# Kernel tuning notes

Measured on AMD Instinct MI355X. Metric: run time of the kernel, lower is better.

## Reference

```python
import jax, jax.numpy as jnp
import numpy as np
from jax import lax

B, V, C, D, H, W = 1, 5, 32, 48, 128, 160
RATIO = 8


def setup_inputs() -> dict:
    key = jax.random.key(0)
    k1, k2, k3 = jax.random.split(key, 3)
    features = jax.random.normal(k1, (V, B, C, H, W), jnp.float32)
    # proj_matrices[b, v, 0] = 4x4 extrinsic, proj_matrices[b, v, 1, :3, :3] = intrinsic K
    f = 200.0
    K = np.array([[f, 0.0, W / 2.0], [0.0, f, H / 2.0], [0.0, 0.0, 1.0]], np.float32)
    proj = np.zeros((B, V, 2, 4, 4), np.float32)
    for v in range(V):
        E = np.eye(4, dtype=np.float32)
        E[0, 3] = 2.0 * v  # horizontal baseline per source view
        proj[:, v, 0] = E
        P1 = np.eye(4, dtype=np.float32)
        P1[:3, :3] = K
        proj[:, v, 1] = P1
    proj_matrices = jnp.asarray(proj)
    depth_values = jnp.broadcast_to(jnp.linspace(425.0, 935.0, D, dtype=jnp.float32), (B, D))
    mask = jax.random.normal(k2, (B, 9 * RATIO * RATIO, H, W), jnp.float32)
    W_reg = jax.random.normal(k3, (1, C, 3, 3, 3), jnp.float32) * 0.05
    return {"features": features, "proj_matrices": proj_matrices,
            "depth_values": depth_values, "mask": mask, "W_reg": W_reg}


def _combine(p):
    # p: [B,2,4,4] -> K @ E[:3,:4] written into top 3 rows of extrinsic (as in source)
    top = jnp.einsum('bij,bjk->bik', p[:, 1, :3, :3], p[:, 0, :3, :4])
    return p[:, 0].at[:, :3, :4].set(top)


def _bilinear_sample(src, x, y):
    # src [B,C,H,W]; x,y [B,P] pixel coords; zeros padding, align_corners=True
    Bs, Cs, Hs, Ws = src.shape
    x0 = jnp.floor(x)
    y0 = jnp.floor(y)
    wx = x - x0
    wy = y - y0
    src_flat = src.reshape(Bs, Cs, Hs * Ws)

    def gather(xi, yi, w):
        valid = (xi >= 0) & (xi <= Ws - 1) & (yi >= 0) & (yi <= Hs - 1)
        xi_c = jnp.clip(xi, 0, Ws - 1).astype(jnp.int32)
        yi_c = jnp.clip(yi, 0, Hs - 1).astype(jnp.int32)
        idx = (yi_c * Ws + xi_c)[:, None, :]
        vals = jnp.take_along_axis(src_flat, jnp.broadcast_to(idx, (Bs, Cs, idx.shape[-1])), axis=2)
        return vals * (w * valid)[:, None, :]

    return (gather(x0, y0, (1 - wx) * (1 - wy)) + gather(x0 + 1, y0, wx * (1 - wy))
            + gather(x0, y0 + 1, (1 - wx) * wy) + gather(x0 + 1, y0 + 1, wx * wy))


def _homo_warp(src_fea, src_proj, ref_proj, depth_values):
    # faithful homo_warping2: project ref pixel grid at each depth hypothesis into src view
    Bs, Cs, Hs, Ws = src_fea.shape
    Dd = depth_values.shape[1]
    proj = jnp.einsum('bij,bjk->bik', src_proj, jnp.linalg.inv(ref_proj))
    rot = proj[:, :3, :3]
    trans = proj[:, :3, 3]
    ys, xs = jnp.meshgrid(jnp.arange(Hs, dtype=src_fea.dtype), jnp.arange(Ws, dtype=src_fea.dtype), indexing='ij')
    xyz = jnp.stack([xs.ravel(), ys.ravel(), jnp.ones(Hs * Ws, dtype=src_fea.dtype)])  # [3,HW]
    rot_xyz = jnp.einsum('bij,jp->bip', rot, xyz)  # [B,3,HW]
    pts = rot_xyz[:, :, None, :] * depth_values[:, None, :, None] + trans[:, :, None, None]  # [B,3,D,HW]
    gx = pts[:, 0] / pts[:, 2]
    gy = pts[:, 1] / pts[:, 2]
    warped = _bilinear_sample(src_fea, gx.reshape(Bs, -1), gy.reshape(Bs, -1))
    return warped.reshape(Bs, Cs, Dd, Hs, Ws)


def _convex_upsample(depth, mask, r):
    # depth [N,1,H,W], mask [N,9*r*r,H,W] -> [N, r*H, r*W]
    N, _, Hh, Ww = depth.shape
    m = jax.nn.softmax(mask.reshape(N, 1, 9, r, r, Hh, Ww), axis=2)
    dp = jnp.pad(depth, ((0, 0), (0, 0), (1, 1), (1, 1)))
    nb = jnp.stack([dp[:, :, dy:dy + Hh, dx:dx + Ww] for dy in range(3) for dx in range(3)], axis=2)
    up = jnp.sum(m * nb[:, :, :, None, None], axis=2)  # [N,1,r,r,H,W]
    up = up.transpose(0, 1, 4, 2, 5, 3)  # [N,1,H,r,W,r]
    return up.reshape(N, r * Hh, r * Ww)


def reference(features, proj_matrices, depth_values, mask, W_reg):
    num_views = features.shape[0]
    Dd = depth_values.shape[1]
    ref_proj = _combine(proj_matrices[:, 0])
    # variance cost-volume accumulation over views (ref volume broadcast along D)
    vsum = features[0][:, :, None, :, :]
    vsq = vsum ** 2
    for v in range(1, num_views):
        src_proj = _combine(proj_matrices[:, v])
        wv = _homo_warp(features[v], src_proj, ref_proj, depth_values)
        vsum = vsum + wv
        vsq = vsq + wv * wv
    variance = vsq / num_views - (vsum / num_views) ** 2  # [B,C,D,H,W]
    # cost regularization stand-in: 3x3x3 conv C->1, SAME padding
    pre = lax.conv_general_dilated(variance, W_reg, (1, 1, 1), 'SAME',
                                   dimension_numbers=('NCDHW', 'OIDHW', 'NCDHW'))[:, 0]
    prob = jax.nn.softmax(pre, axis=1)  # [B,D,H,W]
    depth = jnp.sum(prob * depth_values[:, :, None, None], axis=1)  # [B,H,W]
    # photometric confidence (no-grad path): sliding sum of 4 along D, pad (1,2)
    pd = jnp.pad(prob, ((0, 0), (1, 2), (0, 0), (0, 0)))
    sum4 = pd[:, 0:Dd] + pd[:, 1:Dd + 1] + pd[:, 2:Dd + 2] + pd[:, 3:Dd + 3]
    di = jnp.sum(prob * jnp.arange(Dd, dtype=prob.dtype)[None, :, None, None], axis=1).astype(jnp.int32)
    di = jnp.clip(di, 0, Dd - 1)
    conf = jax.lax.stop_gradient(jnp.take_along_axis(sum4, di[:, None], axis=1)[:, 0])
    depth_up = _convex_upsample(depth[:, None], mask, RATIO)
    return (depth_up, depth, conf)
```

## Files before the change

### kernel.cpp

```cpp
#include <hip/hip_runtime.h>
#include <hip/hip_bf16.h>


#define NV 5
#define NC 32
#define ND 48
#define NH 128
#define NW 160
#define HW (NH * NW)
#define DHW (ND * HW)

typedef __attribute__((ext_vector_type(2))) float f32x2;

#define OFF_M      0
#define OFF_WF     256
#define OFF_DEPTHF 4096
#define OFF_PRE    86016
#define OFF_WV     4018176

__global__ void k_setup(const float* __restrict__ proj,
                        const float* __restrict__ wreg,
                        float* __restrict__ M, float* __restrict__ wf) {
  if (threadIdx.x != 0) return;
  double P[NV][2][4][4];
  for (int v = 0; v < NV; ++v)
    for (int m = 0; m < 2; ++m)
      for (int i = 0; i < 4; ++i)
        for (int j = 0; j < 4; ++j)
          P[v][m][i][j] = (double)proj[((v * 2 + m) * 4 + i) * 4 + j];
  double C[NV][4][4];
  for (int v = 0; v < NV; ++v) {
    for (int i = 0; i < 4; ++i)
      for (int j = 0; j < 4; ++j) C[v][i][j] = P[v][0][i][j];
    for (int i = 0; i < 3; ++i)
      for (int j = 0; j < 4; ++j) {
        double s = 0.0;
        for (int k = 0; k < 3; ++k) s += P[v][1][i][k] * P[v][0][k][j];
        C[v][i][j] = s;
      }
  }
  double a[4][8];
  for (int i = 0; i < 4; ++i)
    for (int j = 0; j < 4; ++j) { a[i][j] = C[0][i][j]; a[i][j + 4] = (i == j) ? 1.0 : 0.0; }
  for (int col = 0; col < 4; ++col) {
    int piv = col; double best = fabs(a[col][col]);
    for (int r = col + 1; r < 4; ++r) { double v = fabs(a[r][col]); if (v > best) { best = v; piv = r; } }
    if (piv != col)
      for (int j = 0; j < 8; ++j) { double t = a[col][j]; a[col][j] = a[piv][j]; a[piv][j] = t; }
    double pv = a[col][col];
    for (int j = 0; j < 8; ++j) a[col][j] /= pv;
    for (int r = 0; r < 4; ++r) if (r != col) {
      double f = a[r][col];
      for (int j = 0; j < 8; ++j) a[r][j] -= f * a[col][j];
    }
  }
  double inv[4][4];
  for (int i = 0; i < 4; ++i)
    for (int j = 0; j < 4; ++j) inv[i][j] = a[i][j + 4];
  for (int v = 1; v < NV; ++v) {
    float* m = M + (v - 1) * 12;
    for (int i = 0; i < 3; ++i) {
      double r[4] = {0, 0, 0, 0};
      for (int k = 0; k < 4; ++k) {
        double cv = C[v][i][k];
        for (int j = 0; j < 4; ++j) r[j] += cv * inv[k][j];
      }
      m[i * 3 + 0] = (float)r[0]; m[i * 3 + 1] = (float)r[1]; m[i * 3 + 2] = (float)r[2];
      m[9 + i] = (float)r[3];
    }
  }
  for (int c = 0; c < NC; ++c) {
    for (int t = 0; t < 27; ++t) wf[c * 28 + t] = wreg[c * 27 + t];
    wf[c * 28 + 27] = 0.f;
  }
}

__global__ __launch_bounds__(256) void k_warpvar(
    const float* __restrict__ feat,
    const float* __restrict__ depthv,
    const float* __restrict__ M,
    const float* __restrict__ wf,
    __hip_bfloat16* __restrict__ WV)
{
  int idx = blockIdx.x * 256 + threadIdx.x;
  int x = idx % NW;
  int t1 = idx / NW;
  int y = t1 % NH;
  int d = t1 / NH;
  float xf = (float)x, yf = (float)y;
  float df = depthv[d];

  int   cidx[16];
  float cw[16];
#pragma unroll
  for (int v = 0; v < 4; ++v) {
    const float* m = M + v * 12;
    float rx = m[0] * xf + m[1] * yf + m[2];
    float ry = m[3] * xf + m[4] * yf + m[5];
    float rz = m[6] * xf + m[7] * yf + m[8];
    float px = rx * df + m[9];
    float py = ry * df + m[10];
    float pz = rz * df + m[11];
    float gx = px / pz;
    float gy = py / pz;
    float x0 = floorf(gx), y0 = floorf(gy);
    float wx = gx - x0, wy = gy - y0;
    float cxs[2] = {x0, x0 + 1.f}, cys[2] = {y0, y0 + 1.f};
    float wxs[2] = {1.f - wx, wx}, wys[2] = {1.f - wy, wy};
#pragma unroll
    for (int cy = 0; cy < 2; ++cy)
#pragma unroll
      for (int cx = 0; cx < 2; ++cx) {
        float fx = cxs[cx], fy = cys[cy];
        bool valid = (fx >= 0.f) && (fx <= (float)(NW - 1)) &&
                     (fy >= 0.f) && (fy <= (float)(NH - 1));
        float fxc = fminf(fmaxf(fx, 0.f), (float)(NW - 1));
        float fyc = fminf(fmaxf(fy, 0.f), (float)(NH - 1));
        int xi = (int)fxc, yi = (int)fyc;
        cidx[v * 4 + cy * 2 + cx] = yi * NW + xi;
        cw[v * 4 + cy * 2 + cx] = wxs[cx] * wys[cy] * (valid ? 1.f : 0.f);
      }
  }

  int pix = y * NW + x;
  f32x2 wv[14];
#pragma unroll
  for (int u = 0; u < 14; ++u) wv[u] = (f32x2){0.f, 0.f};

#pragma unroll
  for (int c = 0; c < NC; ++c) {
    float f0 = feat[c * HW + pix];
    float vs = f0, vq = f0 * f0;
#pragma unroll
    for (int v = 0; v < 4; ++v) {
      const float* fv = feat + ((v + 1) * NC + c) * HW;
      float val = cw[v * 4 + 0] * fv[cidx[v * 4 + 0]]
                + cw[v * 4 + 1] * fv[cidx[v * 4 + 1]]
                + cw[v * 4 + 2] * fv[cidx[v * 4 + 2]]
                + cw[v * 4 + 3] * fv[cidx[v * 4 + 3]];
      vs += val;
      vq += val * val;
    }
    float var = vq * 0.2f - (vs * 0.2f) * (vs * 0.2f);
    const f32x2* wrow = (const f32x2*)(wf + c * 28);
    f32x2 vv; vv.x = var; vv.y = var;
#pragma unroll
    for (int u = 0; u < 14; ++u) wv[u] += wrow[u] * vv;
  }

#pragma unroll
  for (int u = 0; u < 14; ++u) {
    int t0 = 2 * u;
    WV[t0 * DHW + idx] = __float2bfloat16(wv[u].x);
    if (t0 + 1 < 27) WV[(t0 + 1) * DHW + idx] = __float2bfloat16(wv[u].y);
  }
}

__global__ __launch_bounds__(256) void k_conv(const __hip_bfloat16* __restrict__ WV,
                                              float* __restrict__ pre) {
  int idx = blockIdx.x * 256 + threadIdx.x;
  int x = idx % NW;
  int t1 = idx / NW;
  int y = t1 % NH;
  int d = t1 / NH;
  float acc = 0.f;
#pragma unroll
  for (int dd = 0; dd < 3; ++dd) {
    int dp = d + dd - 1;
    bool dok = (dp >= 0) && (dp < ND);
    int dpc = min(max(dp, 0), ND - 1);
#pragma unroll
    for (int i = 0; i < 3; ++i) {
      int yp = y + i - 1;
      bool yok = (yp >= 0) && (yp < NH);
      int ypc = min(max(yp, 0), NH - 1);
#pragma unroll
      for (int j = 0; j < 3; ++j) {
        int xp = x + j - 1;
        bool xok = (xp >= 0) && (xp < NW);
        int xpc = min(max(xp, 0), NW - 1);
        int t = dd * 9 + i * 3 + j;
        float v = __bfloat162float(WV[t * DHW + dpc * HW + ypc * NW + xpc]);
        acc += (dok && yok && xok) ? v : 0.f;
      }
    }
  }
  pre[idx] = acc;
}

__global__ __launch_bounds__(256) void k_softmax(const float* __restrict__ pre,
                                                 const float* __restrict__ depthv,
                                                 float* __restrict__ depthf,
                                                 float* __restrict__ out_depth,
                                                 float* __restrict__ out_conf) {
  int p = blockIdx.x * 256 + threadIdx.x;
  float pr[ND];
  float m = -1e30f;
#pragma unroll
  for (int d = 0; d < ND; ++d) { pr[d] = pre[d * HW + p]; m = fmaxf(m, pr[d]); }
  float s = 0.f;
#pragma unroll
  for (int d = 0; d < ND; ++d) { pr[d] = expf(pr[d] - m); s += pr[d]; }
  float inv = 1.f / s;
  float dep = 0.f, ti = 0.f;
#pragma unroll
  for (int d = 0; d < ND; ++d) {
    float prob = pr[d] * inv;
    pr[d] = prob;
    dep += prob * depthv[d];
    ti += prob * (float)d;
  }
  int di = (int)ti;
  di = di < 0 ? 0 : (di > ND - 1 ? ND - 1 : di);
  float conf = 0.f;
#pragma unroll
  for (int d = 0; d < ND; ++d)
    conf += (d >= di - 1 && d <= di + 2) ? pr[d] : 0.f;
  depthf[p] = dep;
  out_depth[p] = dep;
  out_conf[p] = conf;
}

__global__ __launch_bounds__(256) void k_upsample(const float* __restrict__ mask,
                                                  const float* __restrict__ depthf,
                                                  float* __restrict__ out) {
  int idx = blockIdx.x * 256 + threadIdx.x;
  int fx = idx % (NW * 8);
  int fy = idx / (NW * 8);
  int x = fx >> 3, dx = fx & 7;
  int y = fy >> 3, dy = fy & 7;
  float mv[9];
  float mmax = -1e30f;
#pragma unroll
  for (int k = 0; k < 9; ++k) {
    mv[k] = mask[((k * 8 + dy) * 8 + dx) * HW + y * NW + x];
    mmax = fmaxf(mmax, mv[k]);
  }
  float s = 0.f;
#pragma unroll
  for (int k = 0; k < 9; ++k) { mv[k] = expf(mv[k] - mmax); s += mv[k]; }
  float acc = 0.f;
#pragma unroll
  for (int k = 0; k < 9; ++k) {
    int ky = y + k / 3 - 1;
    int kx = x + k % 3 - 1;
    bool ok = (ky >= 0) && (ky < NH) && (kx >= 0) && (kx < NW);
    int kyc = min(max(ky, 0), NH - 1);
    int kxc = min(max(kx, 0), NW - 1);
    float dv = depthf[kyc * NW + kxc];
    acc += mv[k] * (ok ? dv : 0.f);
  }
  out[idx] = acc / s;
}

extern "C" void kernel_launch(void* const* d_in, const int* in_sizes, int n_in,
                              void* d_out, int out_size, void* d_ws, size_t ws_size,
                              hipStream_t stream) {
  const float* feat   = (const float*)d_in[0];
  const float* proj   = (const float*)d_in[1];
  const float* depthv = (const float*)d_in[2];
  const float* mask   = (const float*)d_in[3];
  const float* wreg   = (const float*)d_in[4];

  char* ws = (char*)d_ws;
  float* M       = (float*)(ws + OFF_M);
  float* wf      = (float*)(ws + OFF_WF);
  float* depthf  = (float*)(ws + OFF_DEPTHF);
  float* pre     = (float*)(ws + OFF_PRE);
  __hip_bfloat16* WV = (__hip_bfloat16*)(ws + OFF_WV);

  float* out = (float*)d_out;
  float* out_depth = out + (NH * 8) * (NW * 8);
  float* out_conf  = out_depth + HW;

  k_setup<<<1, 64, 0, stream>>>(proj, wreg, M, wf);
  k_warpvar<<<DHW / 256, 256, 0, stream>>>(feat, depthv, M, wf, WV);
  k_conv<<<DHW / 256, 256, 0, stream>>>(WV, pre);
  k_softmax<<<HW / 256, 256, 0, stream>>>(pre, depthv, depthf, out_depth, out_conf);
  k_upsample<<<(NH * 8 * NW * 8) / 256, 256, 0, stream>>>(mask, depthf, out);
}
```

Baseline: 275.7 us.

## Pair bilinear taps into 2-wide loads and coalesce upsample mask reads

In the warp/variance kernel, the four bilinear corner gathers per view become two unaligned 2-float loads, one per row. Out-of-range edge cases are handled by moving weights between the left and right slots. This halves the gather instruction count in the dominant kernel. The upsample kernel is also restructured: each block handles one output row and maps threads so mask reads are contiguous in x, then stages results in shared memory for coalesced stores. This adds a block barrier and relies on the edge-case weight remapping being correct.

```diff
diff --git a/kernel.cpp b/kernel.cpp
--- a/kernel.cpp
+++ b/kernel.cpp
@@ -11,6 +11,7 @@
 #define DHW (ND * HW)
 
 typedef __attribute__((ext_vector_type(2))) float f32x2;
+typedef __attribute__((ext_vector_type(2), aligned(4))) float f32x2u;
 
 #define OFF_M      0
 #define OFF_WF     256
@@ -90,8 +91,8 @@
   float xf = (float)x, yf = (float)y;
   float df = depthv[d];
 
-  int   cidx[16];
-  float cw[16];
+  int   r0i[4], r1i[4];
+  float W00[4], W10[4], W01[4], W11[4];
 #pragma unroll
   for (int v = 0; v < 4; ++v) {
     const float* m = M + v * 12;
@@ -103,29 +104,33 @@
     float pz = rz * df + m[11];
     float gx = px / pz;
     float gy = py / pz;
-    float x0 = floorf(gx), y0 = floorf(gy);
-    float wx = gx - x0, wy = gy - y0;
-    float cxs[2] = {x0, x0 + 1.f}, cys[2] = {y0, y0 + 1.f};
-    float wxs[2] = {1.f - wx, wx}, wys[2] = {1.f - wy, wy};
-#pragma unroll
-    for (int cy = 0; cy < 2; ++cy)
-#pragma unroll
-      for (int cx = 0; cx < 2; ++cx) {
-        float fx = cxs[cx], fy = cys[cy];
-        bool valid = (fx >= 0.f) && (fx <= (float)(NW - 1)) &&
-                     (fy >= 0.f) && (fy <= (float)(NH - 1));
-        float fxc = fminf(fmaxf(fx, 0.f), (float)(NW - 1));
-        float fyc = fminf(fmaxf(fy, 0.f), (float)(NH - 1));
-        int xi = (int)fxc, yi = (int)fyc;
-        cidx[v * 4 + cy * 2 + cx] = yi * NW + xi;
-        cw[v * 4 + cy * 2 + cx] = wxs[cx] * wys[cy] * (valid ? 1.f : 0.f);
-      }
+    float x0f = floorf(gx), y0f = floorf(gy);
+    float wx = gx - x0f, wy = gy - y0f;
+    float vx0 = (x0f >= 0.f && x0f <= (float)(NW - 1)) ? 1.f : 0.f;
+    float vx1 = (x0f + 1.f >= 0.f && x0f + 1.f <= (float)(NW - 1)) ? 1.f : 0.f;
+    float vy0 = (y0f >= 0.f && y0f <= (float)(NH - 1)) ? 1.f : 0.f;
+    float vy1 = (y0f + 1.f >= 0.f && y0f + 1.f <= (float)(NH - 1)) ? 1.f : 0.f;
+    float xbf = fminf(fmaxf(x0f, 0.f), (float)(NW - 2));
+    int xb = (int)xbf;
+    float wl = (1.f - wx) * vx0;
+    float wr = wx * vx1;
+    bool leftIsP1 = (x0f > (float)(NW - 2));
+    bool rightIsP0 = (x0f < 0.f);
+    float ax = (leftIsP1 ? 0.f : wl) + (rightIsP0 ? wr : 0.f);
+    float bx = (leftIsP1 ? wl : 0.f) + (rightIsP0 ? 0.f : wr);
+    float yb0f = fminf(fmaxf(y0f, 0.f), (float)(NH - 1));
+    float yb1f = fminf(fmaxf(y0f + 1.f, 0.f), (float)(NH - 1));
+    r0i[v] = (int)yb0f * NW + xb;
+    r1i[v] = (int)yb1f * NW + xb;
+    float wy0 = (1.f - wy) * vy0, wy1 = wy * vy1;
+    W00[v] = ax * wy0; W10[v] = bx * wy0;
+    W01[v] = ax * wy1; W11[v] = bx * wy1;
   }
 
   int pix = y * NW + x;
-  f32x2 wv[14];
-#pragma unroll
-  for (int u = 0; u < 14; ++u) wv[u] = (f32x2){0.f, 0.f};
+  f32x2 wv2[14];
+#pragma unroll
+  for (int u = 0; u < 14; ++u) wv2[u] = (f32x2){0.f, 0.f};
 
 #pragma unroll
   for (int c = 0; c < NC; ++c) {
@@ -133,11 +138,11 @@
     float vs = f0, vq = f0 * f0;
 #pragma unroll
     for (int v = 0; v < 4; ++v) {
-      const float* fv = feat + ((v + 1) * NC + c) * HW;
-      float val = cw[v * 4 + 0] * fv[cidx[v * 4 + 0]]
-                + cw[v * 4 + 1] * fv[cidx[v * 4 + 1]]
-                + cw[v * 4 + 2] * fv[cidx[v * 4 + 2]]
-                + cw[v * 4 + 3] * fv[cidx[v * 4 + 3]];
+      const float* fv = feat + ((size_t)((v + 1) * NC + c)) * HW;
+      f32x2u q0 = *(const f32x2u*)(fv + r0i[v]);
+      f32x2u q1 = *(const f32x2u*)(fv + r1i[v]);
+      float val = W00[v] * q0.x + W10[v] * q0.y
+                + W01[v] * q1.x + W11[v] * q1.y;
       vs += val;
       vq += val * val;
     }
@@ -145,14 +150,14 @@
     const f32x2* wrow = (const f32x2*)(wf + c * 28);
     f32x2 vv; vv.x = var; vv.y = var;
 #pragma unroll
-    for (int u = 0; u < 14; ++u) wv[u] += wrow[u] * vv;
+    for (int u = 0; u < 14; ++u) wv2[u] += wrow[u] * vv;
   }
 
 #pragma unroll
   for (int u = 0; u < 14; ++u) {
     int t0 = 2 * u;
-    WV[t0 * DHW + idx] = __float2bfloat16(wv[u].x);
-    if (t0 + 1 < 27) WV[(t0 + 1) * DHW + idx] = __float2bfloat16(wv[u].y);
+    WV[(size_t)t0 * DHW + idx] = __float2bfloat16(wv2[u].x);
+    if (t0 + 1 < 27) WV[(size_t)(t0 + 1) * DHW + idx] = __float2bfloat16(wv2[u].y);
   }
 }
 
@@ -180,7 +185,7 @@
         bool xok = (xp >= 0) && (xp < NW);
         int xpc = min(max(xp, 0), NW - 1);
         int t = dd * 9 + i * 3 + j;
-        float v = __bfloat162float(WV[t * DHW + dpc * HW + ypc * NW + xpc]);
+        float v = __bfloat162float(WV[(size_t)t * DHW + dpc * HW + ypc * NW + xpc]);
         acc += (dok && yok && xok) ? v : 0.f;
       }
     }
@@ -221,36 +226,47 @@
   out_conf[p] = conf;
 }
 
-__global__ __launch_bounds__(256) void k_upsample(const float* __restrict__ mask,
+__global__ __launch_bounds__(640) void k_upsample(const float* __restrict__ mask,
                                                   const float* __restrict__ depthf,
                                                   float* __restrict__ out) {
-  int idx = blockIdx.x * 256 + threadIdx.x;
-  int fx = idx % (NW * 8);
-  int fy = idx / (NW * 8);
-  int x = fx >> 3, dx = fx & 7;
-  int y = fy >> 3, dy = fy & 7;
-  float mv[9];
-  float mmax = -1e30f;
-#pragma unroll
-  for (int k = 0; k < 9; ++k) {
-    mv[k] = mask[((k * 8 + dy) * 8 + dx) * HW + y * NW + x];
-    mmax = fmaxf(mmax, mv[k]);
-  }
-  float s = 0.f;
-#pragma unroll
-  for (int k = 0; k < 9; ++k) { mv[k] = expf(mv[k] - mmax); s += mv[k]; }
-  float acc = 0.f;
-#pragma unroll
-  for (int k = 0; k < 9; ++k) {
-    int ky = y + k / 3 - 1;
-    int kx = x + k % 3 - 1;
-    bool ok = (ky >= 0) && (ky < NH) && (kx >= 0) && (kx < NW);
-    int kyc = min(max(ky, 0), NH - 1);
-    int kxc = min(max(kx, 0), NW - 1);
-    float dv = depthf[kyc * NW + kxc];
-    acc += mv[k] * (ok ? dv : 0.f);
-  }
-  out[idx] = acc / s;
+  __shared__ float row[NW * 8];
+  int y = blockIdx.x >> 3;
+  int dy = blockIdx.x & 7;
+#pragma unroll
+  for (int rep = 0; rep < 2; ++rep) {
+    int lin = rep * 640 + threadIdx.x;
+    int dx = lin / NW;
+    int x = lin % NW;
+    float mv[9];
+    float mmax = -1e30f;
+#pragma unroll
+    for (int k = 0; k < 9; ++k) {
+      mv[k] = mask[(size_t)(k * 64 + dy * 8 + dx) * HW + y * NW + x];
+      mmax = fmaxf(mmax, mv[k]);
+    }
+    float s = 0.f;
+#pragma unroll
+    for (int k = 0; k < 9; ++k) { mv[k] = expf(mv[k] - mmax); s += mv[k]; }
+    float acc = 0.f;
+#pragma unroll
+    for (int k = 0; k < 9; ++k) {
+      int ky = y + k / 3 - 1;
+      int kx = x + k % 3 - 1;
+      bool ok = (ky >= 0) && (ky < NH) && (kx >= 0) && (kx < NW);
+      int kyc = min(max(ky, 0), NH - 1);
+      int kxc = min(max(kx, 0), NW - 1);
+      float dv = depthf[kyc * NW + kxc];
+      acc += mv[k] * (ok ? dv : 0.f);
+    }
+    row[x * 8 + dx] = acc / s;
+  }
+  __syncthreads();
+  float* orow = out + (size_t)(y * 8 + dy) * (NW * 8);
+#pragma unroll
+  for (int rep = 0; rep < 2; ++rep) {
+    int j = rep * 640 + threadIdx.x;
+    orow[j] = row[j];
+  }
 }
 
 extern "C" void kernel_launch(void* const* d_in, const int* in_sizes, int n_in,
@@ -277,5 +293,5 @@
   k_warpvar<<<DHW / 256, 256, 0, stream>>>(feat, depthv, M, wf, WV);
   k_conv<<<DHW / 256, 256, 0, stream>>>(WV, pre);
   k_softmax<<<HW / 256, 256, 0, stream>>>(pre, depthv, depthf, out_depth, out_conf);
-  k_upsample<<<(NH * 8 * NW * 8) / 256, 256, 0, stream>>>(mask, depthf, out);
-}
+  k_upsample<<<NH * 8, 640, 0, stream>>>(mask, depthf, out);
+}
```

Result: no change. 276.4 us (+0.3%).
